# Performance work log

Hardware: AMD Instinct MI355X
Metric: run time of the kernel (lower is better)

## Reference

```python
import jax, jax.numpy as jnp
import numpy as np

N = 50000      # nodes
E = 800000     # edges (avg degree 16)
IN = 128       # in_channels
H = 128        # hidden_channels
K = 20         # n_clusters
ALPHA = 0.2


def _glorot(key, shape):
    lim = float(np.sqrt(6.0 / (shape[0] + shape[1])))
    return jax.random.uniform(key, shape, jnp.float32, -lim, lim)


def setup_inputs() -> dict:
    key = jax.random.key(0)
    ks = jax.random.split(key, 12)
    x = jax.random.normal(ks[0], (N, IN), jnp.float32)
    edge_index = jax.random.randint(ks[1], (2, E), 0, N, dtype=jnp.int64)
    edge_weight = jax.random.uniform(ks[2], (E,), jnp.float32)
    perm = jax.random.permutation(ks[3], N).astype(jnp.int64)
    W1 = _glorot(ks[4], (IN, H)); b1 = jnp.zeros((H,), jnp.float32)
    W2 = _glorot(ks[5], (H, H));  b2 = jnp.zeros((H,), jnp.float32)
    W3 = _glorot(ks[6], (H, H));  b3 = jnp.zeros((H,), jnp.float32)
    W4 = _glorot(ks[7], (H, H));  b4 = jnp.zeros((H,), jnp.float32)
    prelu_a = jnp.full((H,), 0.25, jnp.float32)
    Wc = _glorot(ks[8], (H, IN)); bc = jnp.zeros((IN,), jnp.float32)
    mu = jax.random.normal(ks[9], (K, IN), jnp.float32)
    return dict(x=x, edge_index=edge_index, edge_weight=edge_weight, perm=perm,
                W1=W1, b1=b1, W2=W2, b2=b2, W3=W3, b3=b3, W4=W4, b4=b4,
                prelu_a=prelu_a, Wc=Wc, bc=bc, mu=mu)


def _gcn_norm(src, dst, ew, n):
    # add self-loops (weight 1) + symmetric normalization, PyG gcn_norm
    loop = jnp.arange(n)
    src2 = jnp.concatenate([src, loop])
    dst2 = jnp.concatenate([dst, loop])
    w2 = jnp.concatenate([ew, jnp.ones((n,), ew.dtype)])
    deg = jax.ops.segment_sum(w2, dst2, num_segments=n)
    dinv = jnp.where(deg > 0, jax.lax.rsqrt(deg), 0.0)
    norm = dinv[src2] * w2 * dinv[dst2]
    return src2, dst2, norm


def _gcn_conv(x, W, b, src2, dst2, norm, n):
    h = x @ W                              # [n, out]
    msg = h[src2] * norm[:, None]          # gather + scale
    return jax.ops.segment_sum(msg, dst2, num_segments=n) + b


def reference(x, edge_index, edge_weight, perm, W1, b1, W2, b2, W3, b3, W4, b4,
              prelu_a, Wc, bc, mu):
    n = x.shape[0]
    src, dst = edge_index[0], edge_index[1]
    src2, dst2, norm = _gcn_norm(src, dst, edge_weight, n)

    def encoder(h):
        h = _gcn_conv(h, W1, b1, src2, dst2, norm, n)
        h = _gcn_conv(h, W2, b2, src2, dst2, norm, n)
        h = _gcn_conv(h, W3, b3, src2, dst2, norm, n)
        h = _gcn_conv(h, W4, b4, src2, dst2, norm, n)
        return jnp.where(h >= 0, h, prelu_a * h)  # PReLU

    pos_z = encoder(x)
    neg_z = encoder(x[perm])                       # corruption: permute node rows
    summary = jax.nn.sigmoid(pos_z.mean(axis=0))   # [H]

    x_out = _gcn_conv(pos_z, Wc, bc, src2, dst2, norm, n)  # [N, IN]

    # Student's-t soft assignment: ||x_i - mu_k||^2 via expansion (same math)
    d = (jnp.sum(x_out * x_out, axis=1, keepdims=True)
         + jnp.sum(mu * mu, axis=1)[None, :]
         - 2.0 * (x_out @ mu.T))
    d = jnp.maximum(d, 0.0)
    q = 1.0 / (1.0 + d / ALPHA + 1e-8)
    q = q ** (ALPHA + 1.0) / 2.0
    q = q / jnp.sum(q, axis=1, keepdims=True)
    return pos_z, neg_z, summary, x_out, q
```

## Files before the change

kernel.cpp:

```cpp
#include <hip/hip_runtime.h>
#include <hip/hip_bf16.h>

constexpr int NN = 50000;
constexpr int EE = 800000;
constexpr int C  = 128;
constexpr int KC = 20;
constexpr int NB = (NN + 1023) / 1024;

typedef __attribute__((ext_vector_type(8))) short bf16x8;
typedef __attribute__((ext_vector_type(4))) float f32x4;

__device__ inline unsigned short f2bf(float f) {
    unsigned u = __float_as_uint(f);
    u += 0x7fff + ((u >> 16) & 1);
    return (unsigned short)(u >> 16);
}
__device__ inline float bf2f(unsigned short h) {
    return __uint_as_float(((unsigned)h) << 16);
}


__global__ void k_hist(const int* __restrict__ ei, unsigned* cnt) {
    int e = blockIdx.x * 256 + threadIdx.x;
    if (e >= EE) return;
    atomicAdd(&cnt[ei[EE + e]], 1u);
}

__global__ __launch_bounds__(256) void k_scan1(const unsigned* __restrict__ cnt,
                                               unsigned* __restrict__ bsum) {
    __shared__ unsigned red[256];
    int b = blockIdx.x, t = threadIdx.x;
    int i0 = b * 1024 + t * 4;
    unsigned s = 0;
    #pragma unroll
    for (int j = 0; j < 4; ++j) { int i = i0 + j; s += (i < NN) ? cnt[i] : 0u; }
    red[t] = s; __syncthreads();
    for (int st = 128; st > 0; st >>= 1) { if (t < st) red[t] += red[t + st]; __syncthreads(); }
    if (t == 0) bsum[b] = red[0];
}

__global__ void k_scan2(unsigned* bsum, unsigned* total) {
    int t = threadIdx.x;
    unsigned v = (t < NB) ? bsum[t] : 0u;
    unsigned x = v;
    #pragma unroll
    for (int s = 1; s < 64; s <<= 1) { unsigned u = __shfl_up(x, s, 64); if (t >= s) x += u; }
    if (t < NB) bsum[t] = x - v;
    if (t == 63) *total = x;
}

__global__ __launch_bounds__(256) void k_scan3(const unsigned* __restrict__ cnt,
                                               const unsigned* __restrict__ bsum,
                                               const unsigned* __restrict__ total,
                                               unsigned* __restrict__ off,
                                               unsigned* __restrict__ cursor) {
    __shared__ unsigned wred[4];
    int b = blockIdx.x, t = threadIdx.x, lane = t & 63, wv = t >> 6;
    int i0 = b * 1024 + t * 4;
    unsigned v[4]; unsigned s = 0;
    #pragma unroll
    for (int j = 0; j < 4; ++j) { int i = i0 + j; v[j] = (i < NN) ? cnt[i] : 0u; s += v[j]; }
    unsigned x = s;
    #pragma unroll
    for (int st = 1; st < 64; st <<= 1) { unsigned u = __shfl_up(x, st, 64); if (lane >= st) x += u; }
    if (lane == 63) wred[wv] = x;
    __syncthreads();
    unsigned woff = 0;
    for (int k = 0; k < 4; ++k) if (k < wv) woff += wred[k];
    unsigned excl = bsum[b] + woff + x - s;
    #pragma unroll
    for (int j = 0; j < 4; ++j) {
        int i = i0 + j;
        if (i < NN) { off[i] = excl; cursor[i] = excl; excl += v[j]; }
    }
    if (b == 0 && t == 0) off[NN] = *total;
}

__global__ void k_fill(const int* __restrict__ ei, const float* __restrict__ ew,
                       unsigned* cursor, uint2* __restrict__ em) {
    int e = blockIdx.x * 256 + threadIdx.x;
    if (e >= EE) return;
    int s = ei[e];
    int d = ei[EE + e];
    unsigned p = atomicAdd(&cursor[d], 1u);
    em[p] = make_uint2((unsigned)s, __float_as_uint(ew[e]));
}

__global__ void k_dinv_csr(const unsigned* __restrict__ off,
                           const uint2* __restrict__ em, float* __restrict__ dinv) {
    int i = blockIdx.x * 256 + threadIdx.x;
    if (i >= NN) return;
    unsigned p0 = off[i], p1 = off[i + 1];
    float s = 1.0f;
    for (unsigned p = p0; p < p1; ++p) s += __uint_as_float(em[p].y);
    dinv[i] = (s > 0.f) ? rsqrtf(s) : 0.f;
}

__global__ void k_scale(const unsigned* __restrict__ off, const float* __restrict__ dinv,
                        uint2* __restrict__ em) {
    int i = blockIdx.x * 256 + threadIdx.x;
    if (i >= NN) return;
    float di = dinv[i];
    unsigned p0 = off[i], p1 = off[i + 1];
    for (unsigned p = p0; p < p1; ++p) {
        uint2 e = em[p];
        em[p].y = __float_as_uint(dinv[e.x] * __uint_as_float(e.y) * di);
    }
}


__global__ void k_wsplit(const float* W0, const float* W1, const float* W2,
                         const float* W3, const float* W4,
                         unsigned short* __restrict__ wt) {
    int m = blockIdx.x >> 6;
    const float* W = (m == 0) ? W0 : (m == 1) ? W1 : (m == 2) ? W2 : (m == 3) ? W3 : W4;
    int idx = (blockIdx.x & 63) * 256 + threadIdx.x;
    int k = idx >> 7, j = idx & 127;
    float v = W[idx];
    unsigned short h = f2bf(v);
    unsigned short* hi = wt + (size_t)(2 * m) * C * C;
    unsigned short* lo = wt + (size_t)(2 * m + 1) * C * C;
    hi[j * C + k] = h;
    lo[j * C + k] = f2bf(v - bf2f(h));
}


__global__ __launch_bounds__(256) void k_mm_f32(const float* __restrict__ A,
                                                const unsigned short* __restrict__ Bh,
                                                const unsigned short* __restrict__ Bl,
                                                unsigned short* __restrict__ G) {
    __shared__ unsigned short Ah[64 * 128];
    __shared__ unsigned short Al[64 * 128];
    int tid  = threadIdx.x;
    int lane = tid & 63;
    int wv   = tid >> 6;
    int row0 = blockIdx.x * 64;

    {
        int r  = tid >> 2;
        int c0 = (tid & 3) * 32;
        int gr = row0 + r;
        bool ok = gr < NN;
        const float* src = A + (size_t)(ok ? gr : 0) * C + c0;
        #pragma unroll
        for (int g = 0; g < 4; ++g) {
            float f[8];
            if (ok) {
                *(float4*)&f[0] = *(const float4*)(src + g * 8);
                *(float4*)&f[4] = *(const float4*)(src + g * 8 + 4);
            } else {
                #pragma unroll
                for (int j = 0; j < 8; ++j) f[j] = 0.f;
            }
            union { unsigned short u[8]; uint4 v; } ph, pl;
            #pragma unroll
            for (int j = 0; j < 8; ++j) {
                unsigned short h = f2bf(f[j]);
                ph.u[j] = h;
                pl.u[j] = f2bf(f[j] - bf2f(h));
            }
            int k = c0 + g * 8;
            int byte = (r * 256 + k * 2) ^ ((r & 7) << 4);
            *(uint4*)((char*)Ah + byte) = ph.v;
            *(uint4*)((char*)Al + byte) = pl.v;
        }
    }

    bf16x8 bh[2][4], bl[2][4];
    #pragma unroll
    for (int cf = 0; cf < 2; ++cf) {
        int col = wv * 32 + cf * 16 + (lane & 15);
        #pragma unroll
        for (int kt = 0; kt < 4; ++kt) {
            int k = kt * 32 + (lane >> 4) * 8;
            bh[cf][kt] = *(const bf16x8*)(Bh + (size_t)col * C + k);
            bl[cf][kt] = *(const bf16x8*)(Bl + (size_t)col * C + k);
        }
    }

    __syncthreads();

    f32x4 zero = {0.f, 0.f, 0.f, 0.f};
    f32x4 acc[4][2];
    #pragma unroll
    for (int rf = 0; rf < 4; ++rf)
        #pragma unroll
        for (int cf = 0; cf < 2; ++cf) acc[rf][cf] = zero;

    #pragma unroll
    for (int rf = 0; rf < 4; ++rf) {
        int row = rf * 16 + (lane & 15);
        #pragma unroll
        for (int kt = 0; kt < 4; ++kt) {
            int k = kt * 32 + (lane >> 4) * 8;
            int byte = (row * 256 + k * 2) ^ ((row & 7) << 4);
            bf16x8 ah = *(const bf16x8*)((const char*)Ah + byte);
            bf16x8 al = *(const bf16x8*)((const char*)Al + byte);
            #pragma unroll
            for (int cf = 0; cf < 2; ++cf) {
                acc[rf][cf] = __builtin_amdgcn_mfma_f32_16x16x32_bf16(ah, bh[cf][kt], acc[rf][cf], 0, 0, 0);
                acc[rf][cf] = __builtin_amdgcn_mfma_f32_16x16x32_bf16(al, bh[cf][kt], acc[rf][cf], 0, 0, 0);
                acc[rf][cf] = __builtin_amdgcn_mfma_f32_16x16x32_bf16(ah, bl[cf][kt], acc[rf][cf], 0, 0, 0);
            }
        }
    }

    #pragma unroll
    for (int cf = 0; cf < 2; ++cf) {
        int col = wv * 32 + cf * 16 + (lane & 15);
        #pragma unroll
        for (int rf = 0; rf < 4; ++rf) {
            #pragma unroll
            for (int q = 0; q < 4; ++q) {
                int row = row0 + rf * 16 + (lane >> 4) * 4 + q;
                if (row < NN) G[(size_t)row * C + col] = f2bf(acc[rf][cf][q]);
            }
        }
    }
}


__global__ __launch_bounds__(256) void k_mm2(const unsigned short* __restrict__ Ap,
                                             const unsigned short* __restrict__ An,
                                             const unsigned short* __restrict__ Bh,
                                             const unsigned short* __restrict__ Bl,
                                             unsigned short* __restrict__ Gp,
                                             unsigned short* __restrict__ Gn, int nblk) {
    __shared__ unsigned short Ah[64 * 128];
    int tid  = threadIdx.x;
    int lane = tid & 63;
    int wv   = tid >> 6;
    int chain = blockIdx.x >= nblk;
    int blk   = chain ? blockIdx.x - nblk : blockIdx.x;
    const unsigned short* A = chain ? An : Ap;
    unsigned short*       G = chain ? Gn : Gp;
    int row0 = blk * 64;

    {
        int r  = tid >> 2;
        int c0 = (tid & 3) * 32;
        int gr = row0 + r;
        bool ok = gr < NN;
        const unsigned short* s = A + (size_t)(ok ? gr : 0) * C + c0;
        #pragma unroll
        for (int g = 0; g < 4; ++g) {
            uint4 v = ok ? *(const uint4*)(s + g * 8) : make_uint4(0, 0, 0, 0);
            int k = c0 + g * 8;
            int byte = (r * 256 + k * 2) ^ ((r & 7) << 4);
            *(uint4*)((char*)Ah + byte) = v;
        }
    }

    bf16x8 bh[2][4], bl[2][4];
    #pragma unroll
    for (int cf = 0; cf < 2; ++cf) {
        int col = wv * 32 + cf * 16 + (lane & 15);
        #pragma unroll
        for (int kt = 0; kt < 4; ++kt) {
            int k = kt * 32 + (lane >> 4) * 8;
            bh[cf][kt] = *(const bf16x8*)(Bh + (size_t)col * C + k);
            bl[cf][kt] = *(const bf16x8*)(Bl + (size_t)col * C + k);
        }
    }

    __syncthreads();

    f32x4 zero = {0.f, 0.f, 0.f, 0.f};
    f32x4 acc[4][2];
    #pragma unroll
    for (int rf = 0; rf < 4; ++rf)
        #pragma unroll
        for (int cf = 0; cf < 2; ++cf) acc[rf][cf] = zero;

    #pragma unroll
    for (int rf = 0; rf < 4; ++rf) {
        int row = rf * 16 + (lane & 15);
        #pragma unroll
        for (int kt = 0; kt < 4; ++kt) {
            int k = kt * 32 + (lane >> 4) * 8;
            int byte = (row * 256 + k * 2) ^ ((row & 7) << 4);
            bf16x8 a = *(const bf16x8*)((const char*)Ah + byte);
            #pragma unroll
            for (int cf = 0; cf < 2; ++cf) {
                acc[rf][cf] = __builtin_amdgcn_mfma_f32_16x16x32_bf16(a, bh[cf][kt], acc[rf][cf], 0, 0, 0);
                acc[rf][cf] = __builtin_amdgcn_mfma_f32_16x16x32_bf16(a, bl[cf][kt], acc[rf][cf], 0, 0, 0);
            }
        }
    }

    #pragma unroll
    for (int cf = 0; cf < 2; ++cf) {
        int col = wv * 32 + cf * 16 + (lane & 15);
        #pragma unroll
        for (int rf = 0; rf < 4; ++rf) {
            #pragma unroll
            for (int q = 0; q < 4; ++q) {
                int row = row0 + rf * 16 + (lane >> 4) * 4 + q;
                if (row < NN) G[(size_t)row * C + col] = f2bf(acc[rf][cf][q]);
            }
        }
    }
}


__global__ __launch_bounds__(256) void k_agg2(const unsigned short* __restrict__ Gp,
                                              const unsigned short* __restrict__ Gn,
                                              const int* __restrict__ permN,
                                              const float* __restrict__ dinv,
                                              const unsigned* __restrict__ off,
                                              const uint2* __restrict__ em,
                                              const float* __restrict__ bias,
                                              const float* __restrict__ prelu,
                                              unsigned short* planeP, unsigned short* planeN,
                                              float* fP, float* fN, int nb) {
    __shared__ uint2 sem[4][64];
    int tid   = threadIdx.x;
    int chain = blockIdx.x >= nb;
    int blk   = chain ? blockIdx.x - nb : blockIdx.x;
    int lane  = tid & 63;
    int wid   = tid >> 6;
    int half  = lane >> 5;
    int gg    = (lane >> 4) & 1;
    int il    = lane & 15;
    int l32   = lane & 31;
    int i     = (blk * 4 + wid) * 2 + half;
    bool act  = i < NN;
    const unsigned short* Gsel = chain ? Gn : Gp;
    const int*            prm  = chain ? permN : nullptr;
    const uint4* H4 = (const uint4*)Gsel;

    float a[8];
    {
        int si = act ? (prm ? prm[i] : i) : 0;
        uint4 hv = H4[(size_t)si * 16 + il];
        float dv = act ? dinv[i] : 0.f;
        float sn = (gg == 0) ? dv * dv : 0.f;
        a[0] = __uint_as_float(hv.x << 16) * sn;
        a[1] = __uint_as_float(hv.x & 0xffff0000u) * sn;
        a[2] = __uint_as_float(hv.y << 16) * sn;
        a[3] = __uint_as_float(hv.y & 0xffff0000u) * sn;
        a[4] = __uint_as_float(hv.z << 16) * sn;
        a[5] = __uint_as_float(hv.z & 0xffff0000u) * sn;
        a[6] = __uint_as_float(hv.w << 16) * sn;
        a[7] = __uint_as_float(hv.w & 0xffff0000u) * sn;
    }

    unsigned p0 = 0, p1 = 0;
    if (act) { p0 = off[i]; p1 = off[i + 1]; }
    for (unsigned base = p0; base < p1; base += 32) {
        unsigned rem = p1 - base;
        int cap = rem < 32u ? (int)rem : 32;
        sem[wid][half * 32 + l32] = em[base + ((unsigned)l32 < rem ? (unsigned)l32 : 0u)];
        #pragma unroll 4
        for (int t = gg; t < cap; t += 2) {
            uint2 e = sem[wid][half * 32 + t];
            unsigned sv = e.x;
            if (prm) sv = (unsigned)prm[sv];
            float wv = __uint_as_float(e.y);
            uint4 hv = H4[(size_t)sv * 16 + il];
            a[0] += __uint_as_float(hv.x << 16) * wv;
            a[1] += __uint_as_float(hv.x & 0xffff0000u) * wv;
            a[2] += __uint_as_float(hv.y << 16) * wv;
            a[3] += __uint_as_float(hv.y & 0xffff0000u) * wv;
            a[4] += __uint_as_float(hv.z << 16) * wv;
            a[5] += __uint_as_float(hv.z & 0xffff0000u) * wv;
            a[6] += __uint_as_float(hv.w << 16) * wv;
            a[7] += __uint_as_float(hv.w & 0xffff0000u) * wv;
        }
    }

    #pragma unroll
    for (int j = 0; j < 8; ++j)
        a[j] += __shfl_xor(a[j], 16, 64);

    {
        float bv[8];
        *(float4*)&bv[0] = *(const float4*)(bias + il * 8);
        *(float4*)&bv[4] = *(const float4*)(bias + il * 8 + 4);
        #pragma unroll
        for (int j = 0; j < 8; ++j) a[j] += bv[j];
        if (prelu) {
            float pv[8];
            *(float4*)&pv[0] = *(const float4*)(prelu + il * 8);
            *(float4*)&pv[4] = *(const float4*)(prelu + il * 8 + 4);
            #pragma unroll
            for (int j = 0; j < 8; ++j) a[j] = (a[j] >= 0.f) ? a[j] : pv[j] * a[j];
        }
    }

    unsigned short* plane = chain ? planeN : planeP;
    float*          fo    = chain ? fN : fP;
    if (act) {
        if (gg == 0 && plane) {
            uint4 o;
            o.x = (unsigned)f2bf(a[0]) | ((unsigned)f2bf(a[1]) << 16);
            o.y = (unsigned)f2bf(a[2]) | ((unsigned)f2bf(a[3]) << 16);
            o.z = (unsigned)f2bf(a[4]) | ((unsigned)f2bf(a[5]) << 16);
            o.w = (unsigned)f2bf(a[6]) | ((unsigned)f2bf(a[7]) << 16);
            ((uint4*)plane)[(size_t)i * 16 + il] = o;
        }
        if (fo) {
            if (gg == 0) *(float4*)(fo + (size_t)i * C + il * 8)     = make_float4(a[0], a[1], a[2], a[3]);
            else         *(float4*)(fo + (size_t)i * C + il * 8 + 4) = make_float4(a[4], a[5], a[6], a[7]);
        }
    }
}


__global__ __launch_bounds__(256) void k_sum(const float* __restrict__ pos, float* sumbuf) {
    __shared__ float red[256];
    int t = threadIdx.x;
    int c = t & 127;
    int half = t >> 7;
    float acc = 0.f;
    for (int r = blockIdx.x * 2 + half; r < NN; r += gridDim.x * 2)
        acc += pos[(size_t)r * C + c];
    red[t] = acc;
    __syncthreads();
    if (half == 0) atomicAdd(&sumbuf[c], acc + red[t + 128]);
}

__global__ void k_summary(const float* sumbuf, float* out) {
    int t = threadIdx.x;
    if (t < C) {
        float m = sumbuf[t] * (1.0f / (float)NN);
        out[t] = 1.0f / (1.0f + expf(-m));
    }
}


__global__ __launch_bounds__(256) void k_q(const float* __restrict__ xo,
                                           const float* __restrict__ mu,
                                           float* __restrict__ qout) {
    __shared__ float sx[64][132];
    __shared__ float smu[KC][128];
    __shared__ float smun[KC];
    int tid = threadIdx.x;
    for (int idx = tid; idx < KC * 128; idx += 256)
        smu[idx >> 7][idx & 127] = mu[idx];
    __syncthreads();
    if (tid < KC) {
        float s = 0.f;
        #pragma unroll 4
        for (int j = 0; j < 128; ++j) { float m = smu[tid][j]; s += m * m; }
        smun[tid] = s;
    }
    int n0 = blockIdx.x * 64;
    for (int idx = tid; idx < 64 * 32; idx += 256) {
        int r = idx >> 5;
        int c = (idx & 31) * 4;
        int gr = n0 + r;
        float4 v = make_float4(0.f, 0.f, 0.f, 0.f);
        if (gr < NN) v = *(const float4*)(xo + (size_t)gr * C + c);
        *(float4*)&sx[r][c] = v;
    }
    __syncthreads();
    int lr = tid >> 2;
    int g  = tid & 3;
    int node = n0 + lr;
    if (node < NN) {
        float ss = 0.f;
        #pragma unroll 8
        for (int j = 0; j < 128; ++j) { float x = sx[lr][j]; ss += x * x; }
        float qv[5]; float qs = 0.f;
        #pragma unroll
        for (int kk = 0; kk < 5; ++kk) {
            int k = g * 5 + kk;
            float dot = 0.f;
            #pragma unroll 8
            for (int j = 0; j < 128; ++j) dot += sx[lr][j] * smu[k][j];
            float d = ss + smun[k] - 2.0f * dot;
            d = fmaxf(d, 0.f);
            float q = 1.0f / (1.0f + d * 5.0f + 1e-8f);
            q = powf(q, 1.2f) * 0.5f;
            qv[kk] = q; qs += q;
        }
        qs += __shfl_xor(qs, 1, 64);
        qs += __shfl_xor(qs, 2, 64);
        float inv = 1.0f / qs;
        #pragma unroll
        for (int kk = 0; kk < 5; ++kk)
            qout[(size_t)node * KC + g * 5 + kk] = qv[kk] * inv;
    }
}


extern "C" void kernel_launch(void* const* d_in, const int* in_sizes, int n_in,
                              void* d_out, int out_size, void* d_ws, size_t ws_size,
                              hipStream_t stream) {
    const float* x    = (const float*)d_in[0];
    const int*   ei   = (const int*)d_in[1];
    const float* ew   = (const float*)d_in[2];
    const int*   perm = (const int*)d_in[3];
    const float* W1 = (const float*)d_in[4];  const float* b1 = (const float*)d_in[5];
    const float* W2 = (const float*)d_in[6];  const float* b2 = (const float*)d_in[7];
    const float* W3 = (const float*)d_in[8];  const float* b3 = (const float*)d_in[9];
    const float* W4 = (const float*)d_in[10]; const float* b4 = (const float*)d_in[11];
    const float* prelu_a = (const float*)d_in[12];
    const float* Wc = (const float*)d_in[13]; const float* bc = (const float*)d_in[14];
    const float* mu = (const float*)d_in[15];

    float* out     = (float*)d_out;
    float* pos_z   = out;
    float* neg_z   = out + (size_t)NN * C;
    float* summary = out + (size_t)2 * NN * C;
    float* xout    = summary + C;
    float* qout    = xout + (size_t)NN * C;

    char* w = (char*)d_ws;
    auto carve = [&](size_t bytes) { void* p = (void*)w; w += (bytes + 511) & ~(size_t)511; return p; };
    float*          dinv   = (float*)carve((size_t)NN * 4);
    unsigned*       cnt    = (unsigned*)carve((size_t)(NN + 1) * 4);
    unsigned*       cursor = (unsigned*)carve((size_t)NN * 4);
    unsigned*       bsum   = (unsigned*)carve(256 * 4);
    unsigned*       total  = (unsigned*)carve(64);
    uint2*          em     = (uint2*)carve((size_t)EE * 8);
    float*          sumbuf = (float*)carve(512);
    unsigned short* wt     = (unsigned short*)carve((size_t)5 * 2 * C * C * 2);
    unsigned short* Gp     = (unsigned short*)carve((size_t)NN * C * 2);
    unsigned short* Gn     = (unsigned short*)carve((size_t)NN * C * 2);
    unsigned short* P0     = (unsigned short*)carve((size_t)NN * C * 2);
    unsigned short* P1     = (unsigned short*)carve((size_t)NN * C * 2);
    unsigned short* P2     = (unsigned short*)carve((size_t)NN * C * 2);

    unsigned short* Wh[5], *Wl[5];
    for (int m = 0; m < 5; ++m) {
        Wh[m] = wt + (size_t)(2 * m) * C * C;
        Wl[m] = wt + (size_t)(2 * m + 1) * C * C;
    }

    hipMemsetAsync(cnt, 0, (size_t)(NN + 1) * 4, stream);
    hipMemsetAsync(sumbuf, 0, 512, stream);

    int gE = (EE + 255) / 256, gN = (NN + 255) / 256;

    k_hist <<<gE, 256, 0, stream>>>(ei, cnt);
    k_scan1<<<NB, 256, 0, stream>>>(cnt, bsum);
    k_scan2<<<1, 64, 0, stream>>>(bsum, total);
    k_scan3<<<NB, 256, 0, stream>>>(cnt, bsum, total, cnt, cursor);
    k_fill <<<gE, 256, 0, stream>>>(ei, ew, cursor, em);
    k_dinv_csr<<<gN, 256, 0, stream>>>(cnt, em, dinv);
    k_scale<<<gN, 256, 0, stream>>>(cnt, dinv, em);

    k_wsplit<<<320, 256, 0, stream>>>(W1, W2, W3, W4, Wc, wt);

    int gM = (NN + 63) / 64;
    int gA = (NN + 7) / 8;

    k_mm_f32<<<gM, 256, 0, stream>>>(x, Wh[0], Wl[0], Gp);
    k_agg2<<<2 * gA, 256, 0, stream>>>(Gp, Gp, perm, dinv, cnt, em, b1, nullptr,
                                       P0, P1, nullptr, nullptr, gA);
    k_mm2 <<<2 * gM, 256, 0, stream>>>(P0, P1, Wh[1], Wl[1], Gp, Gn, gM);
    k_agg2<<<2 * gA, 256, 0, stream>>>(Gp, Gn, nullptr, dinv, cnt, em, b2, nullptr,
                                       P0, P1, nullptr, nullptr, gA);
    k_mm2 <<<2 * gM, 256, 0, stream>>>(P0, P1, Wh[2], Wl[2], Gp, Gn, gM);
    k_agg2<<<2 * gA, 256, 0, stream>>>(Gp, Gn, nullptr, dinv, cnt, em, b3, nullptr,
                                       P0, P1, nullptr, nullptr, gA);
    k_mm2 <<<2 * gM, 256, 0, stream>>>(P0, P1, Wh[3], Wl[3], Gp, Gn, gM);
    k_agg2<<<2 * gA, 256, 0, stream>>>(Gp, Gn, nullptr, dinv, cnt, em, b4, prelu_a,
                                       P2, nullptr, pos_z, neg_z, gA);
    k_mm2 <<<gM, 256, 0, stream>>>(P2, P2, Wh[4], Wl[4], Gp, Gn, gM);
    k_agg2<<<gA, 256, 0, stream>>>(Gp, Gp, nullptr, dinv, cnt, em, bc, nullptr,
                                   nullptr, nullptr, xout, nullptr, gA);

    k_sum<<<256, 256, 0, stream>>>(pos_z, sumbuf);
    k_summary<<<1, 128, 0, stream>>>(sumbuf, summary);

    k_q<<<(NN + 63) / 64, 256, 0, stream>>>(xout, mu, qout);
}
```

Before: 595.3 us.

## Store features as column-quarter planes so aggregation gathers fit in cache

Feature matrices are now stored as four planes of 32 columns each, written by the matmul kernels and read by the aggregation kernel. Aggregation runs as separate passes per quarter, so each pass's random-gather working set (N x 64 bytes) is a quarter of the full matrix and more likely to stay in L2/LLC. Within a pass, each row uses 8 edge slots of 4 lanes, with an extra shuffle reduction. The cost is that edge lists and offsets are re-read four times per layer and there are more blocks.

```diff
diff --git a/kernel.cpp b/kernel.cpp
--- a/kernel.cpp
+++ b/kernel.cpp
@@ -6,6 +6,7 @@
 constexpr int C  = 128;
 constexpr int KC = 20;
 constexpr int NB = (NN + 1023) / 1024;
+constexpr size_t QS = (size_t)NN * 32;
 
 typedef __attribute__((ext_vector_type(8))) short bf16x8;
 typedef __attribute__((ext_vector_type(4))) float f32x4;
@@ -208,12 +209,14 @@
     #pragma unroll
     for (int cf = 0; cf < 2; ++cf) {
         int col = wv * 32 + cf * 16 + (lane & 15);
+        int cc  = col & 31;
+        unsigned short* Gq = G + (size_t)(col >> 5) * QS;
         #pragma unroll
         for (int rf = 0; rf < 4; ++rf) {
             #pragma unroll
             for (int q = 0; q < 4; ++q) {
                 int row = row0 + rf * 16 + (lane >> 4) * 4 + q;
-                if (row < NN) G[(size_t)row * C + col] = f2bf(acc[rf][cf][q]);
+                if (row < NN) Gq[(size_t)row * 32 + cc] = f2bf(acc[rf][cf][q]);
             }
         }
     }
@@ -238,14 +241,15 @@
 
     {
         int r  = tid >> 2;
-        int c0 = (tid & 3) * 32;
+        int qa = tid & 3;
         int gr = row0 + r;
         bool ok = gr < NN;
-        const unsigned short* s = A + (size_t)(ok ? gr : 0) * C + c0;
+        const uint4* Aq = (const uint4*)(A + (size_t)qa * QS);
+        size_t base = (size_t)(ok ? gr : 0) * 4;
         #pragma unroll
         for (int g = 0; g < 4; ++g) {
-            uint4 v = ok ? *(const uint4*)(s + g * 8) : make_uint4(0, 0, 0, 0);
-            int k = c0 + g * 8;
+            uint4 v = ok ? Aq[base + g] : make_uint4(0, 0, 0, 0);
+            int k = qa * 32 + g * 8;
             int byte = (r * 256 + k * 2) ^ ((r & 7) << 4);
             *(uint4*)((char*)Ah + byte) = v;
         }
@@ -291,19 +295,22 @@
     #pragma unroll
     for (int cf = 0; cf < 2; ++cf) {
         int col = wv * 32 + cf * 16 + (lane & 15);
+        int cc  = col & 31;
+        unsigned short* Gq = G + (size_t)(col >> 5) * QS;
         #pragma unroll
         for (int rf = 0; rf < 4; ++rf) {
             #pragma unroll
             for (int q = 0; q < 4; ++q) {
                 int row = row0 + rf * 16 + (lane >> 4) * 4 + q;
-                if (row < NN) G[(size_t)row * C + col] = f2bf(acc[rf][cf][q]);
+                if (row < NN) Gq[(size_t)row * 32 + cc] = f2bf(acc[rf][cf][q]);
             }
         }
     }
 }
 
 
-__global__ __launch_bounds__(256) void k_agg2(const unsigned short* __restrict__ Gp,
+template<int NCHAIN>
+__global__ __launch_bounds__(256) void k_aggq(const unsigned short* __restrict__ Gp,
                                               const unsigned short* __restrict__ Gn,
                                               const int* __restrict__ permN,
                                               const float* __restrict__ dinv,
@@ -314,27 +321,31 @@
                                               unsigned short* planeP, unsigned short* planeN,
                                               float* fP, float* fN, int nb) {
     __shared__ uint2 sem[4][64];
-    int tid   = threadIdx.x;
-    int chain = blockIdx.x >= nb;
-    int blk   = chain ? blockIdx.x - nb : blockIdx.x;
-    int lane  = tid & 63;
-    int wid   = tid >> 6;
-    int half  = lane >> 5;
-    int gg    = (lane >> 4) & 1;
-    int il    = lane & 15;
-    int l32   = lane & 31;
-    int i     = (blk * 4 + wid) * 2 + half;
-    bool act  = i < NN;
+    int tid    = threadIdx.x;
+    int bid    = blockIdx.x;
+    int phase  = bid / nb;
+    int within = bid - phase * nb;
+    int qq, chain;
+    if (NCHAIN == 2) { qq = phase >> 1; chain = phase & 1; }
+    else             { qq = phase;      chain = 0; }
+    int lane = tid & 63;
+    int wid  = tid >> 6;
+    int half = lane >> 5;
+    int l32  = lane & 31;
+    int slot = l32 >> 2;
+    int il4  = lane & 3;
+    int i    = within * 8 + wid * 2 + half;
+    bool act = i < NN;
     const unsigned short* Gsel = chain ? Gn : Gp;
     const int*            prm  = chain ? permN : nullptr;
-    const uint4* H4 = (const uint4*)Gsel;
+    const uint4* H4 = (const uint4*)(Gsel + (size_t)qq * QS);
 
     float a[8];
     {
         int si = act ? (prm ? prm[i] : i) : 0;
-        uint4 hv = H4[(size_t)si * 16 + il];
+        uint4 hv = H4[(size_t)si * 4 + il4];
         float dv = act ? dinv[i] : 0.f;
-        float sn = (gg == 0) ? dv * dv : 0.f;
+        float sn = (slot == 0) ? dv * dv : 0.f;
         a[0] = __uint_as_float(hv.x << 16) * sn;
         a[1] = __uint_as_float(hv.x & 0xffff0000u) * sn;
         a[2] = __uint_as_float(hv.y << 16) * sn;
@@ -351,13 +362,13 @@
         unsigned rem = p1 - base;
         int cap = rem < 32u ? (int)rem : 32;
         sem[wid][half * 32 + l32] = em[base + ((unsigned)l32 < rem ? (unsigned)l32 : 0u)];
-        #pragma unroll 4
-        for (int t = gg; t < cap; t += 2) {
+        #pragma unroll 2
+        for (int t = slot; t < cap; t += 8) {
             uint2 e = sem[wid][half * 32 + t];
             unsigned sv = e.x;
             if (prm) sv = (unsigned)prm[sv];
             float wv = __uint_as_float(e.y);
-            uint4 hv = H4[(size_t)sv * 16 + il];
+            uint4 hv = H4[(size_t)sv * 4 + il4];
             a[0] += __uint_as_float(hv.x << 16) * wv;
             a[1] += __uint_as_float(hv.x & 0xffff0000u) * wv;
             a[2] += __uint_as_float(hv.y << 16) * wv;
@@ -370,38 +381,43 @@
     }
 
     #pragma unroll
-    for (int j = 0; j < 8; ++j)
+    for (int j = 0; j < 8; ++j) {
+        a[j] += __shfl_xor(a[j], 4, 64);
+        a[j] += __shfl_xor(a[j], 8, 64);
         a[j] += __shfl_xor(a[j], 16, 64);
+    }
 
     {
+        int cb = qq * 32 + il4 * 8;
         float bv[8];
-        *(float4*)&bv[0] = *(const float4*)(bias + il * 8);
-        *(float4*)&bv[4] = *(const float4*)(bias + il * 8 + 4);
+        *(float4*)&bv[0] = *(const float4*)(bias + cb);
+        *(float4*)&bv[4] = *(const float4*)(bias + cb + 4);
         #pragma unroll
         for (int j = 0; j < 8; ++j) a[j] += bv[j];
         if (prelu) {
             float pv[8];
-            *(float4*)&pv[0] = *(const float4*)(prelu + il * 8);
-            *(float4*)&pv[4] = *(const float4*)(prelu + il * 8 + 4);
+            *(float4*)&pv[0] = *(const float4*)(prelu + cb);
+            *(float4*)&pv[4] = *(const float4*)(prelu + cb + 4);
             #pragma unroll
             for (int j = 0; j < 8; ++j) a[j] = (a[j] >= 0.f) ? a[j] : pv[j] * a[j];
         }
     }
 
-    unsigned short* plane = chain ? planeN : planeP;
-    float*          fo    = chain ? fN : fP;
-    if (act) {
-        if (gg == 0 && plane) {
+    if (act && slot == 0) {
+        unsigned short* plane = chain ? planeN : planeP;
+        float*          fo    = chain ? fN : fP;
+        if (plane) {
             uint4 o;
             o.x = (unsigned)f2bf(a[0]) | ((unsigned)f2bf(a[1]) << 16);
             o.y = (unsigned)f2bf(a[2]) | ((unsigned)f2bf(a[3]) << 16);
             o.z = (unsigned)f2bf(a[4]) | ((unsigned)f2bf(a[5]) << 16);
             o.w = (unsigned)f2bf(a[6]) | ((unsigned)f2bf(a[7]) << 16);
-            ((uint4*)plane)[(size_t)i * 16 + il] = o;
+            ((uint4*)(plane + (size_t)qq * QS))[(size_t)i * 4 + il4] = o;
         }
         if (fo) {
-            if (gg == 0) *(float4*)(fo + (size_t)i * C + il * 8)     = make_float4(a[0], a[1], a[2], a[3]);
-            else         *(float4*)(fo + (size_t)i * C + il * 8 + 4) = make_float4(a[4], a[5], a[6], a[7]);
+            float* dst = fo + (size_t)i * C + qq * 32 + il4 * 8;
+            *(float4*)dst       = make_float4(a[0], a[1], a[2], a[3]);
+            *(float4*)(dst + 4) = make_float4(a[4], a[5], a[6], a[7]);
         }
     }
 }
@@ -545,23 +561,23 @@
     k_wsplit<<<320, 256, 0, stream>>>(W1, W2, W3, W4, Wc, wt);
 
     int gM = (NN + 63) / 64;
-    int gA = (NN + 7) / 8;
+    int gQ = (NN + 7) / 8;
 
     k_mm_f32<<<gM, 256, 0, stream>>>(x, Wh[0], Wl[0], Gp);
-    k_agg2<<<2 * gA, 256, 0, stream>>>(Gp, Gp, perm, dinv, cnt, em, b1, nullptr,
-                                       P0, P1, nullptr, nullptr, gA);
+    k_aggq<2><<<8 * gQ, 256, 0, stream>>>(Gp, Gp, perm, dinv, cnt, em, b1, nullptr,
+                                          P0, P1, nullptr, nullptr, gQ);
     k_mm2 <<<2 * gM, 256, 0, stream>>>(P0, P1, Wh[1], Wl[1], Gp, Gn, gM);
-    k_agg2<<<2 * gA, 256, 0, stream>>>(Gp, Gn, nullptr, dinv, cnt, em, b2, nullptr,
-                                       P0, P1, nullptr, nullptr, gA);
+    k_aggq<2><<<8 * gQ, 256, 0, stream>>>(Gp, Gn, nullptr, dinv, cnt, em, b2, nullptr,
+                                          P0, P1, nullptr, nullptr, gQ);
     k_mm2 <<<2 * gM, 256, 0, stream>>>(P0, P1, Wh[2], Wl[2], Gp, Gn, gM);
-    k_agg2<<<2 * gA, 256, 0, stream>>>(Gp, Gn, nullptr, dinv, cnt, em, b3, nullptr,
-                                       P0, P1, nullptr, nullptr, gA);
+    k_aggq<2><<<8 * gQ, 256, 0, stream>>>(Gp, Gn, nullptr, dinv, cnt, em, b3, nullptr,
+                                          P0, P1, nullptr, nullptr, gQ);
     k_mm2 <<<2 * gM, 256, 0, stream>>>(P0, P1, Wh[3], Wl[3], Gp, Gn, gM);
-    k_agg2<<<2 * gA, 256, 0, stream>>>(Gp, Gn, nullptr, dinv, cnt, em, b4, prelu_a,
-                                       P2, nullptr, pos_z, neg_z, gA);
+    k_aggq<2><<<8 * gQ, 256, 0, stream>>>(Gp, Gn, nullptr, dinv, cnt, em, b4, prelu_a,
+                                          P2, nullptr, pos_z, neg_z, gQ);
     k_mm2 <<<gM, 256, 0, stream>>>(P2, P2, Wh[4], Wl[4], Gp, Gn, gM);
-    k_agg2<<<gA, 256, 0, stream>>>(Gp, Gp, nullptr, dinv, cnt, em, bc, nullptr,
-                                   nullptr, nullptr, xout, nullptr, gA);
+    k_aggq<1><<<4 * gQ, 256, 0, stream>>>(Gp, Gp, nullptr, dinv, cnt, em, bc, nullptr,
+                                          nullptr, nullptr, xout, nullptr, gQ);
 
     k_sum<<<256, 256, 0, stream>>>(pos_z, sumbuf);
     k_summary<<<1, 128, 0, stream>>>(sumbuf, summary);
```

After: 715.0 us. 20.1% more time.
